# Kernel optimization log

Measured on AMD Instinct MI355X. Metric: run time of the kernel, lower is better.

Reference implementation:

```python
import jax, jax.numpy as jnp
import numpy as np

STRIDE = (1, 1)
PADDING = ((1, 1), (1, 1))  # symmetric padding of 1 on H and W
DILATION = (1, 1)


def setup_inputs() -> dict:
    key = jax.random.key(0)
    k1, k2 = jax.random.split(key)
    x = jax.random.normal(k1, (32, 128, 56, 56), dtype=jnp.float32)
    weight = jax.random.normal(k2, (256, 128, 3, 3), dtype=jnp.float32) * 0.05
    return {"x": x, "weight": weight}


def reference(x, weight):
    # Faithful math of the im2col + matmul conv: identical to a standard
    # cross-correlation Conv2d with stride=1, padding=1, dilation=1, groups=1,
    # bias=False. Expressed as a single fused conv instead of the python-loop
    # gather + stacked GEMM of the original (same output values).
    out = jax.lax.conv_general_dilated(
        x, weight,
        window_strides=STRIDE,
        padding=PADDING,
        rhs_dilation=DILATION,
        dimension_numbers=("NCHW", "OIHW", "NCHW"),
        feature_group_count=1,
    )
    return out  # [B, C_out, H_out, W_out] = [32, 256, 56, 56]
```

## Files before the change

### kernel.cpp

```cpp
#include <hip/hip_runtime.h>
#include <stdint.h>


#define CIN   128
#define HW_   56
#define CO_   256
#define KSZ   1152
#define IMGHW 3136
#define HP    58
#define NT    36
#define XT_BYTES ((size_t)32 * HP * HP * CIN * 2)
#define WP_BYTES ((size_t)CO_ * KSZ * 2)
#define WS_NEED  (XT_BYTES + WP_BYTES)
#define XBLKS    (32 * HP)
#define PBLKS    ((CO_ * KSZ) / 256)

typedef __attribute__((ext_vector_type(8)))  __bf16 bf16x8;
typedef __attribute__((ext_vector_type(4)))  float  f32x4;
typedef __attribute__((ext_vector_type(8)))  unsigned short ushort8;

__device__ __forceinline__ unsigned short f2bf(float f) {
    unsigned int u = __float_as_uint(f);
    u += 0x7fffu + ((u >> 16) & 1u);
    return (unsigned short)(u >> 16);
}

__device__ __forceinline__ void gl2lds16(const void* g, void* l) {
    __builtin_amdgcn_global_load_lds(
        (const __attribute__((address_space(1))) void*)g,
        (__attribute__((address_space(3))) void*)l, 16, 0, 0);
}

__global__ __launch_bounds__(256)
void prep(const float* __restrict__ x, unsigned short* __restrict__ xt,
          const float* __restrict__ w, unsigned short* __restrict__ wp2) {
    const int t = threadIdx.x;
    if (blockIdx.x >= XBLKS) {
        int o = (blockIdx.x - XBLKS) * 256 + t;
        int e    = o & 7;
        int lane = (o >> 3) & 63;
        int cog  = (o >> 9) & 15;
        int tt   = o >> 13;
        int co = cog * 16 + (lane & 15);
        int k  = tt * 32 + (lane >> 4) * 8 + e;
        wp2[o] = f2bf(w[(co * CIN + (k & 127)) * 9 + (k >> 7)]);
        return;
    }
    const int nb = blockIdx.x;
    const int n  = nb / HP;
    const int hp = nb - n * HP;
    unsigned short* orow = xt + ((size_t)n * HP + hp) * (HP * CIN);

    if (hp == 0 || hp == HP - 1) {
        for (int i = t; i < (HP * CIN) / 8; i += 256)
            ((ushort8*)orow)[i] = (ushort8){0, 0, 0, 0, 0, 0, 0, 0};
        return;
    }
    const int h = hp - 1;
    __shared__ ushort2 T[CIN][31];
    {
        const int ci = t >> 1, part = t & 1;
        const float* src = x + (((size_t)n * CIN + ci) * IMGHW + h * HW_ + part * 28);
        #pragma unroll
        for (int j = 0; j < 7; ++j) {
            float4 v = *(const float4*)(src + 4 * j);
            T[ci][part * 14 + 2 * j]     = (ushort2){f2bf(v.x), f2bf(v.y)};
            T[ci][part * 14 + 2 * j + 1] = (ushort2){f2bf(v.z), f2bf(v.w)};
        }
    }
    __syncthreads();
    const int wpg = t >> 4, cig = t & 15;
    const int ci0 = cig * 8;
    for (int wp_ = wpg; wp_ < HP; wp_ += 16) {
        ushort8 v = (ushort8){0, 0, 0, 0, 0, 0, 0, 0};
        const int w_ = wp_ - 1;
        if ((unsigned)w_ < (unsigned)HW_) {
            #pragma unroll
            for (int e = 0; e < 8; ++e) {
                ushort2 p = T[ci0 + e][w_ >> 1];
                v[e] = (w_ & 1) ? p.y : p.x;
            }
        }
        *(ushort8*)(orow + wp_ * CIN + ci0) = v;
    }
}

__global__ __launch_bounds__(256, 2)
void conv14(const unsigned short* __restrict__ xt,
            const unsigned short* __restrict__ wp2,
            float* __restrict__ out)
{
    __shared__ __align__(16) char lds[2][16384];

    const int tid  = threadIdx.x;
    const int lane = tid & 63;
    const int wid  = tid >> 6;

    int bid = blockIdx.x;
    int flat = (bid & 7) * 98 + (bid >> 3);
    const int mt_ = flat >> 1;
    const int n0  = (flat & 1) << 7;
    const int m0  = mt_ << 8;

    const int lc = (tid & 7) ^ ((tid >> 3) & 7);
    uint32_t aoff[4];
    #pragma unroll
    for (int p = 0; p < 4; ++p) {
        int m = m0 + ((p * 32 + (tid >> 3)) << 1) + (lc >> 2);
        int n = m / IMGHW;
        int rem = m - n * IMGHW;
        int h = rem / HW_;
        int w = rem - h * HW_;
        aoff[p] = (uint32_t)((((n * HP + h) * HP + w) << 8) + ((lc & 3) << 4));
    }

    const int fr = lane & 15, fg = lane >> 4;
    const int cp = (((fr & 1) << 2) | fg) ^ ((fr >> 1) & 7);
    const int wm0 = (wid >> 1) << 7;
    const int wn0 = (wid & 1) << 6;
    const int aB = (((wm0 >> 1) + (fr >> 1)) << 7) + (cp << 4);

    const int nfgB = (n0 + wn0) >> 4;
    const unsigned short* wpb = wp2 + (size_t)lane * 8;

    const char* xtc = (const char*)xt;

    f32x4 acc[8][4];
    #pragma unroll
    for (int i = 0; i < 8; ++i)
        #pragma unroll
        for (int j = 0; j < 4; ++j)
            acc[i][j] = (f32x4){0.f, 0.f, 0.f, 0.f};

    ushort8 b0r[4], b1r[4];

    auto STAGE = [&](int t) {
        char* L = &lds[t & 1][0];
        int tap = t >> 2;
        int kh = (tap * 11) >> 5;
        int kw = tap - kh * 3;
        uint32_t asl = (uint32_t)(((kh * HP + kw) << 8) + ((t & 3) << 6));
        #pragma unroll
        for (int p = 0; p < 4; ++p)
            gl2lds16(xtc + aoff[p] + asl, L + p * 4096 + tid * 16);
    };

    #define LOADB(B_, t) do { \
        _Pragma("unroll") for (int nf_ = 0; nf_ < 4; ++nf_) \
            B_[nf_] = *(const ushort8*)(wpb + \
                (size_t)(((t) * 16 + nfgB + nf_) * 64) * 8); \
    } while (0)

    #define TILE(t, BC, BN) do { \
        if ((t) + 1 < NT) { \
            STAGE((t) + 1); \
            __builtin_amdgcn_sched_barrier(0); \
            LOADB(BN, (t) + 1); \
            __builtin_amdgcn_sched_barrier(0); \
        } \
        const char* L_ = &lds[(t) & 1][0]; \
        ushort8 a_[8]; \
        _Pragma("unroll") for (int mf_ = 0; mf_ < 8; ++mf_) \
            a_[mf_] = *(const ushort8*)(L_ + aB + mf_ * 1024); \
        __builtin_amdgcn_s_setprio(1); \
        _Pragma("unroll") for (int mf_ = 0; mf_ < 8; ++mf_) \
            _Pragma("unroll") for (int nf_ = 0; nf_ < 4; ++nf_) \
                acc[mf_][nf_] = __builtin_amdgcn_mfma_f32_16x16x32_bf16( \
                    __builtin_bit_cast(bf16x8, BC[nf_]), \
                    __builtin_bit_cast(bf16x8, a_[mf_]), \
                    acc[mf_][nf_], 0, 0, 0); \
        __builtin_amdgcn_s_setprio(0); \
        if ((t) + 1 < NT) \
            asm volatile("s_waitcnt vmcnt(0)" ::: "memory"); \
        __builtin_amdgcn_s_barrier(); \
    } while (0)

    STAGE(0);
    LOADB(b0r, 0);
    asm volatile("s_waitcnt vmcnt(0)" ::: "memory");
    __builtin_amdgcn_s_barrier();

    #pragma unroll 1
    for (int tt = 0; tt < NT; tt += 2) {
        TILE(tt, b0r, b1r);
        TILE(tt + 1, b1r, b0r);
    }

    const int mwave = m0 + wm0;
    const int co0 = n0 + wn0 + (fg << 2);
    #pragma unroll
    for (int mf = 0; mf < 8; ++mf) {
        int m = mwave + mf * 16 + fr;
        int n = m / IMGHW;
        int hwr = m - n * IMGHW;
        uint32_t basem = (uint32_t)(n * (CO_ * IMGHW) + hwr);
        #pragma unroll
        for (int nf = 0; nf < 4; ++nf)
            #pragma unroll
            for (int q = 0; q < 4; ++q)
                out[basem + (uint32_t)(co0 + nf * 16 + q) * IMGHW] = acc[mf][nf][q];
    }
    #undef LOADB
    #undef TILE
}

#define BM    64
#define BK    32
#define NSTEP 36
#define LDSP  40

template<bool PACKED>
__global__ __launch_bounds__(256, 2)
void conv_fb(const float* __restrict__ x,
             const float* __restrict__ wraw,
             const unsigned short* __restrict__ wp,
             float* __restrict__ out)
{
    __shared__ __align__(16) unsigned short Al[2][BM][LDSP];
    __shared__ __align__(16) unsigned short Bl[2][CO_][LDSP];

    const int tid  = threadIdx.x;
    const int lane = tid & 63;
    const int wid  = tid >> 6;

    const int mb    = blockIdx.x;
    const int n_img = mb / 49;
    const int hw0   = (mb - n_img * 49) * BM;

    const int mm = lane;
    const int hw = hw0 + mm;
    const int h  = hw / HW_;
    const int w_ = hw - h * HW_;

    const int bco  = tid >> 2;
    const int bkkg = tid & 3;

    float   aPF[8];
    ushort8 bPF[4];

    auto loadA = [&](int step) {
        int khkw = step >> 2;
        int kh = khkw / 3, kw = khkw - (khkw / 3) * 3;
        int ci0 = (step & 3) * BK + wid * 8;
        int ih = h + kh - 1, iw = w_ + kw - 1;
        bool valid = ((unsigned)ih < (unsigned)HW_) && ((unsigned)iw < (unsigned)HW_);
        const float* px = x + (((size_t)(n_img * CIN + ci0) * HW_ + ih) * HW_ + iw);
        #pragma unroll
        for (int e = 0; e < 8; ++e)
            aPF[e] = valid ? px[e * IMGHW] : 0.f;
    };
    auto writeA = [&](int buf) {
        ushort8 v;
        #pragma unroll
        for (int e = 0; e < 8; ++e) v[e] = f2bf(aPF[e]);
        *(ushort8*)&Al[buf][mm][wid * 8] = v;
    };
    auto loadB = [&](int step) {
        int khkw = step >> 2;
        int ci0 = (step & 3) * BK + bkkg * 8;
        #pragma unroll
        for (int r = 0; r < 4; ++r) {
            int co = r * 64 + bco;
            ushort8 v;
            #pragma unroll
            for (int e = 0; e < 8; ++e)
                v[e] = f2bf(wraw[(co * CIN + ci0 + e) * 9 + khkw]);
            bPF[r] = v;
        }
    };
    auto writeB = [&](int buf) {
        #pragma unroll
        for (int r = 0; r < 4; ++r)
            *(ushort8*)&Bl[buf][r * 64 + bco][bkkg * 8] = bPF[r];
    };

    f32x4 acc[4][4];
    #pragma unroll
    for (int i = 0; i < 4; ++i)
        #pragma unroll
        for (int j = 0; j < 4; ++j)
            acc[i][j] = (f32x4){0.f, 0.f, 0.f, 0.f};

    const int frow = lane & 15;
    const int fk   = (lane >> 4) * 8;

    loadA(0); loadB(0);
    writeA(0); writeB(0);
    __syncthreads();

    for (int s = 0; s < NSTEP; ++s) {
        const int cur = s & 1;
        if (s + 1 < NSTEP) { loadA(s + 1); loadB(s + 1); }

        ushort8 aF[4], bF[4];
        #pragma unroll
        for (int i = 0; i < 4; ++i)
            aF[i] = *(const ushort8*)&Bl[cur][wid * 64 + i * 16 + frow][fk];
        #pragma unroll
        for (int j = 0; j < 4; ++j)
            bF[j] = *(const ushort8*)&Al[cur][j * 16 + frow][fk];

        #pragma unroll
        for (int i = 0; i < 4; ++i)
            #pragma unroll
            for (int j = 0; j < 4; ++j)
                acc[i][j] = __builtin_amdgcn_mfma_f32_16x16x32_bf16(
                    __builtin_bit_cast(bf16x8, aF[i]),
                    __builtin_bit_cast(bf16x8, bF[j]),
                    acc[i][j], 0, 0, 0);

        if (s + 1 < NSTEP) { writeA(cur ^ 1); writeB(cur ^ 1); }
        __syncthreads();
    }

    float* ob = out + (size_t)n_img * (CO_ * IMGHW) + hw0;
    #pragma unroll
    for (int i = 0; i < 4; ++i) {
        int co0 = wid * 64 + i * 16 + (lane >> 4) * 4;
        #pragma unroll
        for (int j = 0; j < 4; ++j) {
            int mcol = j * 16 + (lane & 15);
            #pragma unroll
            for (int q = 0; q < 4; ++q)
                ob[(size_t)(co0 + q) * IMGHW + mcol] = acc[i][j][q];
        }
    }
}

extern "C" void kernel_launch(void* const* d_in, const int* in_sizes, int n_in,
                              void* d_out, int out_size, void* d_ws, size_t ws_size,
                              hipStream_t stream) {
    (void)in_sizes; (void)n_in; (void)out_size;
    const float* x  = (const float*)d_in[0];
    const float* wt = (const float*)d_in[1];
    float* out = (float*)d_out;

    if (ws_size >= WS_NEED) {
        unsigned short* xt  = (unsigned short*)d_ws;
        unsigned short* wp2 = (unsigned short*)((char*)d_ws + XT_BYTES);
        prep<<<XBLKS + PBLKS, 256, 0, stream>>>(x, xt, wt, wp2);
        conv14<<<784, 256, 0, stream>>>(xt, wp2, out);
    } else {
        conv_fb<false><<<100352 / BM, 256, 0, stream>>>(x, wt, nullptr, out);
    }
}
```

Baseline: 92.52 us.

## Load conv operands directly from global memory, dropping LDS staging and double buffering

The conv kernel no longer stages the activation tile into LDS through async global-to-LDS copies with double buffering and barriers. Each wave now loads its A fragments and B weights straight from global memory into registers every K step, then issues the MFMAs. This removes the LDS traffic, the barriers and the shared-memory footprint. In exchange, the two waves that share the same rows load them twice, and loads are no longer prefetched ahead of compute, so memory latency is exposed on every step.

```diff
diff --git a/kernel.cpp b/kernel.cpp
--- a/kernel.cpp
+++ b/kernel.cpp
@@ -23,12 +23,6 @@
     unsigned int u = __float_as_uint(f);
     u += 0x7fffu + ((u >> 16) & 1u);
     return (unsigned short)(u >> 16);
-}
-
-__device__ __forceinline__ void gl2lds16(const void* g, void* l) {
-    __builtin_amdgcn_global_load_lds(
-        (const __attribute__((address_space(1))) void*)g,
-        (__attribute__((address_space(3))) void*)l, 16, 0, 0);
 }
 
 __global__ __launch_bounds__(256)
@@ -86,12 +80,10 @@
 }
 
 __global__ __launch_bounds__(256, 2)
-void conv14(const unsigned short* __restrict__ xt,
+void conv15(const unsigned short* __restrict__ xt,
             const unsigned short* __restrict__ wp2,
             float* __restrict__ out)
 {
-    __shared__ __align__(16) char lds[2][16384];
-
     const int tid  = threadIdx.x;
     const int lane = tid & 63;
     const int wid  = tid >> 6;
@@ -102,27 +94,23 @@
     const int n0  = (flat & 1) << 7;
     const int m0  = mt_ << 8;
 
-    const int lc = (tid & 7) ^ ((tid >> 3) & 7);
-    uint32_t aoff[4];
-    #pragma unroll
-    for (int p = 0; p < 4; ++p) {
-        int m = m0 + ((p * 32 + (tid >> 3)) << 1) + (lc >> 2);
+    const int fr = lane & 15, fg = lane >> 4;
+    const int wm0 = (wid >> 1) << 7;
+    const int wn0 = (wid & 1) << 6;
+
+    uint32_t aBase[8];
+    #pragma unroll
+    for (int mf = 0; mf < 8; ++mf) {
+        int m = m0 + wm0 + mf * 16 + fr;
         int n = m / IMGHW;
         int rem = m - n * IMGHW;
         int h = rem / HW_;
         int w = rem - h * HW_;
-        aoff[p] = (uint32_t)((((n * HP + h) * HP + w) << 8) + ((lc & 3) << 4));
-    }
-
-    const int fr = lane & 15, fg = lane >> 4;
-    const int cp = (((fr & 1) << 2) | fg) ^ ((fr >> 1) & 7);
-    const int wm0 = (wid >> 1) << 7;
-    const int wn0 = (wid & 1) << 6;
-    const int aB = (((wm0 >> 1) + (fr >> 1)) << 7) + (cp << 4);
+        aBase[mf] = (uint32_t)((((n * HP + h) * HP + w) << 8) + (fg << 4));
+    }
 
     const int nfgB = (n0 + wn0) >> 4;
     const unsigned short* wpb = wp2 + (size_t)lane * 8;
-
     const char* xtc = (const char*)xt;
 
     f32x4 acc[8][4];
@@ -132,58 +120,29 @@
         for (int j = 0; j < 4; ++j)
             acc[i][j] = (f32x4){0.f, 0.f, 0.f, 0.f};
 
-    ushort8 b0r[4], b1r[4];
-
-    auto STAGE = [&](int t) {
-        char* L = &lds[t & 1][0];
+    #pragma unroll 1
+    for (int t = 0; t < NT; ++t) {
         int tap = t >> 2;
         int kh = (tap * 11) >> 5;
         int kw = tap - kh * 3;
-        uint32_t asl = (uint32_t)(((kh * HP + kw) << 8) + ((t & 3) << 6));
-        #pragma unroll
-        for (int p = 0; p < 4; ++p)
-            gl2lds16(xtc + aoff[p] + asl, L + p * 4096 + tid * 16);
-    };
-
-    #define LOADB(B_, t) do { \
-        _Pragma("unroll") for (int nf_ = 0; nf_ < 4; ++nf_) \
-            B_[nf_] = *(const ushort8*)(wpb + \
-                (size_t)(((t) * 16 + nfgB + nf_) * 64) * 8); \
-    } while (0)
-
-    #define TILE(t, BC, BN) do { \
-        if ((t) + 1 < NT) { \
-            STAGE((t) + 1); \
-            __builtin_amdgcn_sched_barrier(0); \
-            LOADB(BN, (t) + 1); \
-            __builtin_amdgcn_sched_barrier(0); \
-        } \
-        const char* L_ = &lds[(t) & 1][0]; \
-        ushort8 a_[8]; \
-        _Pragma("unroll") for (int mf_ = 0; mf_ < 8; ++mf_) \
-            a_[mf_] = *(const ushort8*)(L_ + aB + mf_ * 1024); \
-        __builtin_amdgcn_s_setprio(1); \
-        _Pragma("unroll") for (int mf_ = 0; mf_ < 8; ++mf_) \
-            _Pragma("unroll") for (int nf_ = 0; nf_ < 4; ++nf_) \
-                acc[mf_][nf_] = __builtin_amdgcn_mfma_f32_16x16x32_bf16( \
-                    __builtin_bit_cast(bf16x8, BC[nf_]), \
-                    __builtin_bit_cast(bf16x8, a_[mf_]), \
-                    acc[mf_][nf_], 0, 0, 0); \
-        __builtin_amdgcn_s_setprio(0); \
-        if ((t) + 1 < NT) \
-            asm volatile("s_waitcnt vmcnt(0)" ::: "memory"); \
-        __builtin_amdgcn_s_barrier(); \
-    } while (0)
-
-    STAGE(0);
-    LOADB(b0r, 0);
-    asm volatile("s_waitcnt vmcnt(0)" ::: "memory");
-    __builtin_amdgcn_s_barrier();
-
-    #pragma unroll 1
-    for (int tt = 0; tt < NT; tt += 2) {
-        TILE(tt, b0r, b1r);
-        TILE(tt + 1, b1r, b0r);
+        const uint32_t asl = (uint32_t)(((kh * HP + kw) << 8) + ((t & 3) << 6));
+
+        ushort8 a[8], b[4];
+        #pragma unroll
+        for (int nf = 0; nf < 4; ++nf)
+            b[nf] = *(const ushort8*)(wpb + (size_t)((t * 16 + nfgB + nf) * 64) * 8);
+        #pragma unroll
+        for (int mf = 0; mf < 8; ++mf)
+            a[mf] = *(const ushort8*)(xtc + aBase[mf] + asl);
+
+        #pragma unroll
+        for (int mf = 0; mf < 8; ++mf)
+            #pragma unroll
+            for (int nf = 0; nf < 4; ++nf)
+                acc[mf][nf] = __builtin_amdgcn_mfma_f32_16x16x32_bf16(
+                    __builtin_bit_cast(bf16x8, b[nf]),
+                    __builtin_bit_cast(bf16x8, a[mf]),
+                    acc[mf][nf], 0, 0, 0);
     }
 
     const int mwave = m0 + wm0;
@@ -200,8 +159,6 @@
             for (int q = 0; q < 4; ++q)
                 out[basem + (uint32_t)(co0 + nf * 16 + q) * IMGHW] = acc[mf][nf][q];
     }
-    #undef LOADB
-    #undef TILE
 }
 
 #define BM    64
@@ -339,7 +296,7 @@
         unsigned short* xt  = (unsigned short*)d_ws;
         unsigned short* wp2 = (unsigned short*)((char*)d_ws + XT_BYTES);
         prep<<<XBLKS + PBLKS, 256, 0, stream>>>(x, xt, wt, wp2);
-        conv14<<<784, 256, 0, stream>>>(xt, wp2, out);
+        conv15<<<784, 256, 0, stream>>>(xt, wp2, out);
     } else {
         conv_fb<false><<<100352 / BM, 256, 0, stream>>>(x, wt, nullptr, out);
     }
```

After: 176.9 us. 1.91x slower.
